# Performance work log

Measured on AMD Instinct MI355X. Metric: run time of the kernel, lower is better.

The kernel has to match this reference:

```python
import jax, jax.numpy as jnp
import numpy as np

SHIFT = 1  # module picks random +/-1 at init; fixed to +1 for determinism


def setup_inputs() -> dict:
    key = jax.random.key(0)
    k1, k2, k3 = jax.random.split(key, 3)
    return {
        "x": jax.random.normal(k1, (1, 24, 56, 56), dtype=jnp.float32),
        "W0": jax.random.normal(k2, (48, 9), dtype=jnp.float32),   # weights[0]
        "W1": jax.random.normal(k3, (12, 7, 9), dtype=jnp.float32),  # weights[1]
    }


def reference(x, W0, W1):
    # x -> (o=2, j=12, n=56, m=56); n is folded into unfold channels,
    # the sliding window (k=7, pad=3) runs over m.
    a = x.reshape(2, 12, 56, 56)
    ap = jnp.pad(a, ((0, 0), (0, 0), (0, 0), (3, 3)))  # pad the windowed axis
    idx = jnp.arange(7)[:, None] + jnp.arange(56)[None, :]  # (k, m) gather indices
    t3 = ap[:, :, :, idx]  # (o, j, n, k, m) == torch (1,2,12,56,7,56) with l=1 dropped
    # einsum('lojnkm, jki -> lonmi')
    t4 = jnp.einsum('ojnkm,jki->onmi', t3, W1)  # (2, 56, 56, 9)
    # einsum('knmli, ji -> knjml') with t4 axes renamed -> (o, p, n, m)
    t5 = jnp.einsum('onmi,pi->opnm', t4, W0)    # (2, 48, 56, 56)
    y = t5.reshape(1, 96, 56, 56)
    return jnp.roll(y, SHIFT, axis=2)
```

## Files before the change

kernel.cpp:

```cpp
#include <hip/hip_runtime.h>
#include <hip/hip_bf16.h>


__global__ __launch_bounds__(64) void fused_shiftconv_kernel(
    const float* __restrict__ x,
    const float* __restrict__ W0,
    const float* __restrict__ W1,
    float* __restrict__ out)
{
    __shared__ float sA[12][62];
    __shared__ float sW1[756];
    __shared__ float sW0[432];
    __shared__ float sT4[56][9];

    const int tid = threadIdx.x;
    const int o = blockIdx.x / 56;
    const int n = blockIdx.x % 56;

    for (int idx = tid; idx < 756; idx += 64) sW1[idx] = W1[idx];
    for (int idx = tid; idx < 432; idx += 64) sW0[idx] = W0[idx];

    for (int idx = tid; idx < 12 * 62; idx += 64) {
        const int j  = idx / 62;
        const int mm = idx % 62;
        const int msrc = mm - 3;
        float v = 0.0f;
        if (msrc >= 0 && msrc < 56)
            v = x[((o * 12 + j) * 56 + n) * 56 + msrc];
        sA[j][mm] = v;
    }
    __syncthreads();

    if (tid < 56) {
        const int m = tid;
        float acc[9];
#pragma unroll
        for (int i = 0; i < 9; ++i) acc[i] = 0.0f;

        for (int j = 0; j < 12; ++j) {
#pragma unroll
            for (int k = 0; k < 7; ++k) {
                const float v = sA[j][m + k];
                const float* w = &sW1[(j * 7 + k) * 9];
#pragma unroll
                for (int i = 0; i < 9; ++i) acc[i] += v * w[i];
            }
        }
#pragma unroll
        for (int i = 0; i < 9; ++i) sT4[m][i] = acc[i];
    }
    __syncthreads();

    const int n_out = (n + 1) % 56;
    for (int idx2 = tid; idx2 < 48 * 56; idx2 += 64) {
        const int p = idx2 / 56;
        const int m = idx2 % 56;
        const float* w = &sW0[p * 9];
        const float* t = &sT4[m][0];
        float acc = 0.0f;
#pragma unroll
        for (int i = 0; i < 9; ++i) acc += w[i] * t[i];
        out[((o * 48 + p) * 56 + n_out) * 56 + m] = acc;
    }
}

extern "C" void kernel_launch(void* const* d_in, const int* in_sizes, int n_in,
                              void* d_out, int out_size, void* d_ws, size_t ws_size,
                              hipStream_t stream) {
    const float* x  = (const float*)d_in[0];
    const float* W0 = (const float*)d_in[1];
    const float* W1 = (const float*)d_in[2];
    float* out = (float*)d_out;

    fused_shiftconv_kernel<<<dim3(112), dim3(64), 0, stream>>>(x, W0, W1, out);
}
```

Baseline: 73.48 us.

## Split channel reduction across four waves and vectorize weight loads and output stores

```diff
diff --git a/kernel.cpp b/kernel.cpp
--- a/kernel.cpp
+++ b/kernel.cpp
@@ -2,65 +2,86 @@
 #include <hip/hip_bf16.h>
 
 
-__global__ __launch_bounds__(64) void fused_shiftconv_kernel(
+__global__ __launch_bounds__(256) void fused_shiftconv_v2(
     const float* __restrict__ x,
     const float* __restrict__ W0,
     const float* __restrict__ W1,
     float* __restrict__ out)
 {
-    __shared__ float sA[12][62];
-    __shared__ float sW1[756];
-    __shared__ float sW0[432];
-    __shared__ float sT4[56][9];
+    __shared__ __align__(16) float sA[12][64];
+    __shared__ __align__(16) float sW1[756];
+    __shared__ __align__(16) float sW0[432];
+    __shared__ __align__(16) float sPart[4][9][60];
+    __shared__ __align__(16) float sT4t[9][60];
 
     const int tid = threadIdx.x;
     const int o = blockIdx.x / 56;
     const int n = blockIdx.x % 56;
 
-    for (int idx = tid; idx < 756; idx += 64) sW1[idx] = W1[idx];
-    for (int idx = tid; idx < 432; idx += 64) sW0[idx] = W0[idx];
+    {
+        const float4* W1v = (const float4*)W1;
+        float4* s1 = (float4*)sW1;
+        for (int idx = tid; idx < 189; idx += 256) s1[idx] = W1v[idx];
+        const float4* W0v = (const float4*)W0;
+        float4* s0 = (float4*)sW0;
+        for (int idx = tid; idx < 108; idx += 256) s0[idx] = W0v[idx];
+    }
 
-    for (int idx = tid; idx < 12 * 62; idx += 64) {
-        const int j  = idx / 62;
-        const int mm = idx % 62;
-        const int msrc = mm - 3;
+    for (int idx = tid; idx < 12 * 64; idx += 256) {
+        const int j = idx >> 6, mm = idx & 63;
+        const int ms = mm - 3;
         float v = 0.0f;
-        if (msrc >= 0 && msrc < 56)
-            v = x[((o * 12 + j) * 56 + n) * 56 + msrc];
+        if (ms >= 0 && ms < 56)
+            v = x[((o * 12 + j) * 56 + n) * 56 + ms];
         sA[j][mm] = v;
     }
     __syncthreads();
 
-    if (tid < 56) {
-        const int m = tid;
-        float acc[9];
+    {
+        const int wave = tid >> 6, lane = tid & 63;
+        if (lane < 56) {
+            const int m = lane;
+            float acc[9];
 #pragma unroll
-        for (int i = 0; i < 9; ++i) acc[i] = 0.0f;
+            for (int i = 0; i < 9; ++i) acc[i] = 0.0f;
+#pragma unroll
+            for (int jj = 0; jj < 3; ++jj) {
+                const int j = wave * 3 + jj;
+#pragma unroll
+                for (int k = 0; k < 7; ++k) {
+                    const float v = sA[j][m + k];
+                    const float* w = &sW1[(j * 7 + k) * 9];
+#pragma unroll
+                    for (int i = 0; i < 9; ++i) acc[i] += v * w[i];
+                }
+            }
+#pragma unroll
+            for (int i = 0; i < 9; ++i) sPart[wave][i][m] = acc[i];
+        }
+    }
+    __syncthreads();
 
-        for (int j = 0; j < 12; ++j) {
-#pragma unroll
-            for (int k = 0; k < 7; ++k) {
-                const float v = sA[j][m + k];
-                const float* w = &sW1[(j * 7 + k) * 9];
-#pragma unroll
-                for (int i = 0; i < 9; ++i) acc[i] += v * w[i];
-            }
-        }
-#pragma unroll
-        for (int i = 0; i < 9; ++i) sT4[m][i] = acc[i];
+    for (int idx = tid; idx < 504; idx += 256) {
+        const int i = idx / 56, m = idx % 56;
+        sT4t[i][m] = sPart[0][i][m] + sPart[1][i][m]
+                   + sPart[2][i][m] + sPart[3][i][m];
     }
     __syncthreads();
 
     const int n_out = (n + 1) % 56;
-    for (int idx2 = tid; idx2 < 48 * 56; idx2 += 64) {
-        const int p = idx2 / 56;
-        const int m = idx2 % 56;
+    for (int v4 = tid; v4 < 672; v4 += 256) {
+        const int p = v4 / 14;
+        const int m0 = (v4 % 14) * 4;
         const float* w = &sW0[p * 9];
-        const float* t = &sT4[m][0];
-        float acc = 0.0f;
+        float4 acc = {0.0f, 0.0f, 0.0f, 0.0f};
 #pragma unroll
-        for (int i = 0; i < 9; ++i) acc += w[i] * t[i];
-        out[((o * 48 + p) * 56 + n_out) * 56 + m] = acc;
+        for (int i = 0; i < 9; ++i) {
+            const float4 t = *(const float4*)&sT4t[i][m0];
+            const float wi = w[i];
+            acc.x += wi * t.x; acc.y += wi * t.y;
+            acc.z += wi * t.z; acc.w += wi * t.w;
+        }
+        *(float4*)&out[((o * 48 + p) * 56 + n_out) * 56 + m0] = acc;
     }
 }
 
@@ -72,5 +93,5 @@
     const float* W1 = (const float*)d_in[2];
     float* out = (float*)d_out;
 
-    fused_shiftconv_kernel<<<dim3(112), dim3(64), 0, stream>>>(x, W0, W1, out);
+    fused_shiftconv_v2<<<dim3(112), dim3(256), 0, stream>>>(x, W0, W1, out);
 }
```

Result: faster. 61.00 us (-17.0%).
